# Performance work log

Hardware: AMD Instinct MI355X
Metric: run time of the kernel (lower is better)

## Reference

```python
import jax, jax.numpy as jnp
import numpy as np

N = 4096
IN_F = 256
OUT_F = 64
K = 4
ALPHA = 0.2  # LeakyReLU negative slope
NEG_INF = -9e15


def setup_inputs() -> dict:
    key = jax.random.key(0)
    k_h, k_w, k_a, k_e, k_m = jax.random.split(key, 5)
    h = jax.random.normal(k_h, (N, IN_F), dtype=jnp.float32)
    # xavier_uniform with gain=1.414
    def xavier(k, shape, gain=1.414):
        fan_in, fan_out = shape[0], shape[1]
        limit = gain * np.sqrt(6.0 / (fan_in + fan_out))
        return jax.random.uniform(k, shape, jnp.float32, -limit, limit)
    W = xavier(k_w, (IN_F, OUT_F))
    a = xavier(k_a, (2 * OUT_F, 1))
    vals = jax.random.uniform(k_e, (K, N, N), dtype=jnp.float32)
    mask = jax.random.uniform(k_m, (K, N, N), dtype=jnp.float32) < 0.05
    edge_attr = jnp.where(mask, vals, 0.0)
    return {"h": h, "edge_attr": edge_attr, "W": W, "a": a}


def reference(h, edge_attr, W, a):
    # h: [N, IN_F], edge_attr: [K, N, N], W: [IN_F, OUT_F], a: [2*OUT_F, 1]
    Wh = h @ W                                   # [N, OUT_F]
    Wh1 = Wh @ a[:OUT_F, :]                      # [N, 1]
    Wh2 = Wh @ a[OUT_F:, :]                      # [N, 1]
    e = jax.nn.leaky_relu(Wh1 + Wh2.T, negative_slope=ALPHA)  # [N, N]
    e = e[None, :, :] * edge_attr                # [K, N, N]
    e = jnp.where(edge_attr > 0, e, NEG_INF)
    att = jax.nn.softmax(e, axis=1)              # softmax over dim=1, as in torch
    # dropout is identity in eval mode
    # batched replacement for the per-channel python loop of matmuls
    hp = jnp.einsum('kij,jf->kif', att, Wh)      # [K, N, OUT_F]
    out = jnp.transpose(hp, (1, 0, 2)).reshape(N, K * OUT_F)  # concat dim=1
    return jax.nn.elu(out), att
```

## Files before the change

### kernel.cpp

```cpp
#include <hip/hip_runtime.h>

#define NN 4096
#define IN_F 256
#define OUT_F 64
#define K_CH 4
#define ALPHA 0.2f
#define JP 16
#define JCOLS 256
#define ROWS1 32
#define IC1 128
#define BSTRIDE 264

typedef __bf16 bf16;
typedef __attribute__((ext_vector_type(8))) __bf16 bf16x8;
typedef __attribute__((ext_vector_type(4))) __bf16 bf16x4;
typedef __attribute__((ext_vector_type(4))) float f32x4;

__global__ __launch_bounds__(256) void k0_wh(const float* __restrict__ h,
                                             const float* __restrict__ W,
                                             const float* __restrict__ a,
                                             float* __restrict__ Wh,
                                             float* __restrict__ Wh1,
                                             float* __restrict__ Wh2) {
    int tid = threadIdx.x;
    int wave = tid >> 6, lane = tid & 63;
    int i = blockIdx.x * 4 + wave;
    const float* hrow = h + (size_t)i * IN_F;
    float acc = 0.f;
    #pragma unroll 8
    for (int c = 0; c < IN_F; ++c)
        acc += hrow[c] * W[c * OUT_F + lane];
    Wh[(size_t)i * OUT_F + lane] = acc;
    float v1 = acc * a[lane];
    float v2 = acc * a[OUT_F + lane];
    #pragma unroll
    for (int o = 32; o > 0; o >>= 1) {
        v1 += __shfl_xor(v1, o, 64);
        v2 += __shfl_xor(v2, o, 64);
    }
    if (lane == 0) { Wh1[i] = v1; Wh2[i] = v2; }
}

__global__ __launch_bounds__(256) void k0_transpose(const float* __restrict__ Wh,
                                                    bf16* __restrict__ WhT) {
    __shared__ float lds[OUT_F * 65];
    int tid = threadIdx.x;
    int i0 = blockIdx.x * 64;
    int f = tid & 63;
    int r0 = tid >> 6;
    #pragma unroll
    for (int s = 0; s < 16; ++s) {
        int r = r0 * 16 + s;
        lds[f * 65 + r] = Wh[(size_t)(i0 + r) * OUT_F + f];
    }
    __syncthreads();
    int f2 = tid >> 2;
    int c0 = (tid & 3) * 16;
    #pragma unroll
    for (int s = 0; s < 16; ++s) {
        int c = c0 + s;
        WhT[(size_t)f2 * NN + i0 + c] = (bf16)lds[f2 * 65 + c];
    }
}

__global__ __launch_bounds__(256) void k1_colsum(const float* __restrict__ edge,
                                                 const float* __restrict__ Wh1,
                                                 const float* __restrict__ Wh2,
                                                 bf16* __restrict__ p_buf,
                                                 float* __restrict__ partial) {
    int tid = threadIdx.x;
    int kch = blockIdx.z;
    int j0 = blockIdx.y * 1024 + tid * 4;
    int ic = blockIdx.x;
    int ibase = ic * ROWS1;
    f32x4 w2 = *(const f32x4*)&Wh2[j0];
    f32x4 s = {0.f, 0.f, 0.f, 0.f};
    const float* base = edge + ((size_t)kch * NN + ibase) * NN + j0;
    bf16* pbase = p_buf + ((size_t)kch * NN + ibase) * NN + j0;
    f32x4 r[8];
    #pragma unroll
    for (int t = 0; t < 8; ++t)
        r[t] = *(const f32x4*)(base + (size_t)t * NN);
    #pragma unroll
    for (int ii = 0; ii < ROWS1; ++ii) {
        int cur = ii & 7;
        f32x4 e = r[cur];
        int ip = (ii + 8 < ROWS1) ? ii + 8 : ii;
        r[cur] = *(const f32x4*)(base + (size_t)ip * NN);
        float wh1 = Wh1[ibase + ii];
        bf16x4 pv;
        #pragma unroll
        for (int c = 0; c < 4; ++c) {
            float xv = wh1 + w2[c];
            float lk = xv > 0.f ? xv : ALPHA * xv;
            float val = e[c] > 0.f ? __expf(lk * e[c]) : 0.f;
            bf16 vb = (bf16)val;
            pv[c] = vb;
            s[c] += (float)vb;
        }
        *(bf16x4*)(pbase + (size_t)ii * NN) = pv;
    }
    *(f32x4*)(partial + ((size_t)kch * IC1 + ic) * NN + j0) = s;
}

__global__ __launch_bounds__(256) void k1_reduce(const float* __restrict__ partial,
                                                 float* __restrict__ s_inv) {
    __shared__ float red[256];
    int tid = threadIdx.x;
    int kch = blockIdx.y;
    int jl = tid & 63, g = tid >> 6;
    int j = blockIdx.x * 64 + jl;
    const float* pb = partial + (size_t)kch * IC1 * NN;
    float s = 0.f;
    #pragma unroll 8
    for (int t = 0; t < IC1 / 4; ++t)
        s += pb[(size_t)(g * (IC1 / 4) + t) * NN + j];
    red[tid] = s;
    __syncthreads();
    if (tid < 64) {
        float tot = red[tid] + red[tid + 64] + red[tid + 128] + red[tid + 192];
        s_inv[kch * NN + j] = tot > 0.f ? 1.f / tot : 0.f;
    }
}

__global__ __launch_bounds__(256) void k2_fused(const bf16* __restrict__ p_buf,
                                                const float* __restrict__ s_inv,
                                                const bf16* __restrict__ WhT,
                                                float* __restrict__ att_out,
                                                float* __restrict__ hp) {
    __shared__ bf16 ldsB[OUT_F * BSTRIDE];
    __shared__ float lds_inv[JCOLS];
    int tid = threadIdx.x;
    int itile = blockIdx.x;
    int z = blockIdx.y;
    int kch = z >> 4, jp = z & 15;
    int jbase0 = jp * JCOLS;
    {
        int f = tid >> 2, part = (tid & 3) * 64;
        #pragma unroll
        for (int u = 0; u < 8; ++u) {
            bf16x8 v = *(const bf16x8*)(WhT + (size_t)f * NN + jbase0 + part + u * 8);
            *(bf16x8*)&ldsB[f * BSTRIDE + part + u * 8] = v;
        }
        lds_inv[tid] = s_inv[kch * NN + jbase0 + tid];
    }
    __syncthreads();
    int wave = tid >> 6, lane = tid & 63;
    int n16 = lane & 15, quad = lane >> 4;
    int i_row = itile * 64 + wave * 16 + n16;
    const size_t ebase = ((size_t)kch * NN + i_row) * NN + jbase0 + quad * 8;
    const bf16* pptr = p_buf + ebase;
    float* aptr = att_out + ebase;
    f32x4 acc[4] = {};
    bf16x8 pf[4];
    #pragma unroll
    for (int t = 0; t < 4; ++t)
        pf[t] = *(const bf16x8*)(pptr + t * 32);
    #pragma unroll
    for (int s = 0; s < JCOLS / 32; ++s) {
        int cur = s & 3;
        bf16x8 pv = pf[cur];
        int sp = (s + 4 < JCOLS / 32) ? s + 4 : s;
        pf[cur] = *(const bf16x8*)(pptr + sp * 32);
        int jl = s * 32 + quad * 8;
        f32x4 iv0 = *(const f32x4*)&lds_inv[jl];
        f32x4 iv1 = *(const f32x4*)&lds_inv[jl + 4];
        bf16x8 afrag;
        f32x4 av0, av1;
        #pragma unroll
        for (int c = 0; c < 8; ++c) {
            float isc = c < 4 ? iv0[c] : iv1[c - 4];
            float attv = (float)pv[c] * isc;
            afrag[c] = (bf16)attv;
            if (c < 4) av0[c] = attv; else av1[c - 4] = attv;
        }
        *(f32x4*)(aptr + s * 32) = av0;
        *(f32x4*)(aptr + s * 32 + 4) = av1;
        #pragma unroll
        for (int ft = 0; ft < 4; ++ft) {
            bf16x8 bfrag = *(const bf16x8*)&ldsB[(ft * 16 + n16) * BSTRIDE + jl];
            acc[ft] = __builtin_amdgcn_mfma_f32_16x16x32_bf16(afrag, bfrag, acc[ft], 0, 0, 0);
        }
    }
    #pragma unroll
    for (int ft = 0; ft < 4; ++ft) {
        #pragma unroll
        for (int r = 0; r < 4; ++r) {
            int row_l = quad * 4 + r;
            int i_g = itile * 64 + wave * 16 + row_l;
            size_t idx = ((size_t)z * NN + i_g) * OUT_F + ft * 16 + n16;
            hp[idx] = acc[ft][r];
        }
    }
}

__global__ __launch_bounds__(256) void k3_combine(const float* __restrict__ hp,
                                                  float* __restrict__ out) {
    int g = blockIdx.x * 256 + threadIdx.x;
    int i = g >> 8;
    int rem = g & 255;
    int kch = rem >> 6;
    int f = rem & 63;
    float s = 0.f;
    #pragma unroll
    for (int z = 0; z < JP; ++z)
        s += hp[(((size_t)(kch * JP + z)) * NN + i) * OUT_F + f];
    out[g] = s > 0.f ? s : __expf(s) - 1.f;
}

extern "C" void kernel_launch(void* const* d_in, const int* in_sizes, int n_in,
                              void* d_out, int out_size, void* d_ws, size_t ws_size,
                              hipStream_t stream) {
    (void)out_size; (void)ws_size;
    const float *h = nullptr, *edge = nullptr, *W = nullptr, *a = nullptr;
    for (int i = 0; i < n_in; ++i) {
        int sz = in_sizes[i];
        if (sz == NN * IN_F)               h    = (const float*)d_in[i];
        else if (sz == K_CH * NN * NN)     edge = (const float*)d_in[i];
        else if (sz == IN_F * OUT_F)       W    = (const float*)d_in[i];
        else if (sz == 2 * OUT_F)          a    = (const float*)d_in[i];
    }

    char* ws = (char*)d_ws;
    size_t off = 0;
    float* Wh      = (float*)(ws + off); off += (size_t)NN * OUT_F * 4;
    float* Wh1     = (float*)(ws + off); off += NN * 4;
    float* Wh2     = (float*)(ws + off); off += NN * 4;
    float* s_inv   = (float*)(ws + off); off += (size_t)K_CH * NN * 4;
    bf16*  WhT     = (bf16*) (ws + off); off += (size_t)OUT_F * NN * 2;
    float* partial = (float*)(ws + off); off += (size_t)K_CH * IC1 * NN * 4;
    float* hp      = (float*)(ws + off); off += (size_t)K_CH * JP * NN * OUT_F * 4;
    bf16*  p_buf   = (bf16*) (ws + off); off += (size_t)K_CH * NN * NN * 2;

    float* out_h   = (float*)d_out;
    float* att_out = out_h + (size_t)NN * (K_CH * OUT_F);

    k0_wh<<<dim3(NN / 4), 256, 0, stream>>>(h, W, a, Wh, Wh1, Wh2);
    k0_transpose<<<dim3(NN / 64), 256, 0, stream>>>(Wh, WhT);
    k1_colsum<<<dim3(IC1, 4, K_CH), 256, 0, stream>>>(edge, Wh1, Wh2, p_buf, partial);
    k1_reduce<<<dim3(NN / 64, K_CH), 256, 0, stream>>>(partial, s_inv);
    k2_fused<<<dim3(64, K_CH * JP), 256, 0, stream>>>(p_buf, s_inv, WhT, att_out, hp);
    k3_combine<<<dim3((NN * K_CH * OUT_F) / 256), 256, 0, stream>>>(hp, out_h);
}
```

Before: 593.9 us.

## Fuse split-j partial reduction and ELU into attention-matmul kernel

The attention-times-Wh kernel now loops over the full j range inside each block, staging Wh^T in 256-column LDS slabs, instead of splitting j across 16 blocks. It applies ELU and writes the final output directly. This removes the large partial-sum hp buffer, its write and read-back traffic, and the separate combine launch. In exchange the grid shrinks from 4096 to 256 blocks, roughly one per CU. That low occupancy, plus the per-slab barriers, may leave the memory-bound attention streaming under-saturated.

```diff
diff --git a/kernel.cpp b/kernel.cpp
--- a/kernel.cpp
+++ b/kernel.cpp
@@ -5,8 +5,6 @@
 #define OUT_F 64
 #define K_CH 4
 #define ALPHA 0.2f
-#define JP 16
-#define JCOLS 256
 #define ROWS1 32
 #define IC1 128
 #define BSTRIDE 264
@@ -127,59 +125,63 @@
                                                 const float* __restrict__ s_inv,
                                                 const bf16* __restrict__ WhT,
                                                 float* __restrict__ att_out,
-                                                float* __restrict__ hp) {
+                                                float* __restrict__ out) {
     __shared__ bf16 ldsB[OUT_F * BSTRIDE];
-    __shared__ float lds_inv[JCOLS];
+    __shared__ float lds_inv[NN];
     int tid = threadIdx.x;
     int itile = blockIdx.x;
-    int z = blockIdx.y;
-    int kch = z >> 4, jp = z & 15;
-    int jbase0 = jp * JCOLS;
-    {
-        int f = tid >> 2, part = (tid & 3) * 64;
-        #pragma unroll
-        for (int u = 0; u < 8; ++u) {
-            bf16x8 v = *(const bf16x8*)(WhT + (size_t)f * NN + jbase0 + part + u * 8);
-            *(bf16x8*)&ldsB[f * BSTRIDE + part + u * 8] = v;
-        }
-        lds_inv[tid] = s_inv[kch * NN + jbase0 + tid];
-    }
-    __syncthreads();
+    int kch = blockIdx.y;
+    #pragma unroll
+    for (int t = 0; t < NN / 256; ++t)
+        lds_inv[t * 256 + tid] = s_inv[kch * NN + t * 256 + tid];
     int wave = tid >> 6, lane = tid & 63;
     int n16 = lane & 15, quad = lane >> 4;
     int i_row = itile * 64 + wave * 16 + n16;
-    const size_t ebase = ((size_t)kch * NN + i_row) * NN + jbase0 + quad * 8;
+    const size_t ebase = ((size_t)kch * NN + i_row) * NN + quad * 8;
     const bf16* pptr = p_buf + ebase;
     float* aptr = att_out + ebase;
     f32x4 acc[4] = {};
-    bf16x8 pf[4];
-    #pragma unroll
-    for (int t = 0; t < 4; ++t)
+    bf16x8 pf[8];
+    #pragma unroll
+    for (int t = 0; t < 8; ++t)
         pf[t] = *(const bf16x8*)(pptr + t * 32);
-    #pragma unroll
-    for (int s = 0; s < JCOLS / 32; ++s) {
-        int cur = s & 3;
-        bf16x8 pv = pf[cur];
-        int sp = (s + 4 < JCOLS / 32) ? s + 4 : s;
-        pf[cur] = *(const bf16x8*)(pptr + sp * 32);
-        int jl = s * 32 + quad * 8;
-        f32x4 iv0 = *(const f32x4*)&lds_inv[jl];
-        f32x4 iv1 = *(const f32x4*)&lds_inv[jl + 4];
-        bf16x8 afrag;
-        f32x4 av0, av1;
-        #pragma unroll
-        for (int c = 0; c < 8; ++c) {
-            float isc = c < 4 ? iv0[c] : iv1[c - 4];
-            float attv = (float)pv[c] * isc;
-            afrag[c] = (bf16)attv;
-            if (c < 4) av0[c] = attv; else av1[c - 4] = attv;
-        }
-        *(f32x4*)(aptr + s * 32) = av0;
-        *(f32x4*)(aptr + s * 32 + 4) = av1;
-        #pragma unroll
-        for (int ft = 0; ft < 4; ++ft) {
-            bf16x8 bfrag = *(const bf16x8*)&ldsB[(ft * 16 + n16) * BSTRIDE + jl];
-            acc[ft] = __builtin_amdgcn_mfma_f32_16x16x32_bf16(afrag, bfrag, acc[ft], 0, 0, 0);
+    int f = tid >> 2, part = (tid & 3) * 64;
+    const bf16* wsrc = WhT + (size_t)f * NN + part;
+    for (int slab = 0; slab < 16; ++slab) {
+        __syncthreads();
+        #pragma unroll
+        for (int u = 0; u < 8; ++u) {
+            bf16x8 v = *(const bf16x8*)(wsrc + slab * 256 + u * 8);
+            *(bf16x8*)&ldsB[f * BSTRIDE + part + u * 8] = v;
+        }
+        __syncthreads();
+        #pragma unroll
+        for (int t = 0; t < 8; ++t) {
+            int g = slab * 8 + t;
+            int cur = g & 7;
+            bf16x8 pv = pf[cur];
+            int gp = (g + 8 < 128) ? g + 8 : g;
+            pf[cur] = *(const bf16x8*)(pptr + gp * 32);
+            int jg = g * 32 + quad * 8;
+            int jl = t * 32 + quad * 8;
+            f32x4 iv0 = *(const f32x4*)&lds_inv[jg];
+            f32x4 iv1 = *(const f32x4*)&lds_inv[jg + 4];
+            bf16x8 afrag;
+            f32x4 av0, av1;
+            #pragma unroll
+            for (int c = 0; c < 8; ++c) {
+                float isc = c < 4 ? iv0[c] : iv1[c - 4];
+                float attv = (float)pv[c] * isc;
+                afrag[c] = (bf16)attv;
+                if (c < 4) av0[c] = attv; else av1[c - 4] = attv;
+            }
+            *(f32x4*)(aptr + g * 32) = av0;
+            *(f32x4*)(aptr + g * 32 + 4) = av1;
+            #pragma unroll
+            for (int ft = 0; ft < 4; ++ft) {
+                bf16x8 bfrag = *(const bf16x8*)&ldsB[(ft * 16 + n16) * BSTRIDE + jl];
+                acc[ft] = __builtin_amdgcn_mfma_f32_16x16x32_bf16(afrag, bfrag, acc[ft], 0, 0, 0);
+            }
         }
     }
     #pragma unroll
@@ -188,24 +190,11 @@
         for (int r = 0; r < 4; ++r) {
             int row_l = quad * 4 + r;
             int i_g = itile * 64 + wave * 16 + row_l;
-            size_t idx = ((size_t)z * NN + i_g) * OUT_F + ft * 16 + n16;
-            hp[idx] = acc[ft][r];
-        }
-    }
-}
-
-__global__ __launch_bounds__(256) void k3_combine(const float* __restrict__ hp,
-                                                  float* __restrict__ out) {
-    int g = blockIdx.x * 256 + threadIdx.x;
-    int i = g >> 8;
-    int rem = g & 255;
-    int kch = rem >> 6;
-    int f = rem & 63;
-    float s = 0.f;
-    #pragma unroll
-    for (int z = 0; z < JP; ++z)
-        s += hp[(((size_t)(kch * JP + z)) * NN + i) * OUT_F + f];
-    out[g] = s > 0.f ? s : __expf(s) - 1.f;
+            float v = acc[ft][r];
+            out[(size_t)i_g * (K_CH * OUT_F) + kch * OUT_F + ft * 16 + n16] =
+                v > 0.f ? v : __expf(v) - 1.f;
+        }
+    }
 }
 
 extern "C" void kernel_launch(void* const* d_in, const int* in_sizes, int n_in,
@@ -229,7 +218,6 @@
     float* s_inv   = (float*)(ws + off); off += (size_t)K_CH * NN * 4;
     bf16*  WhT     = (bf16*) (ws + off); off += (size_t)OUT_F * NN * 2;
     float* partial = (float*)(ws + off); off += (size_t)K_CH * IC1 * NN * 4;
-    float* hp      = (float*)(ws + off); off += (size_t)K_CH * JP * NN * OUT_F * 4;
     bf16*  p_buf   = (bf16*) (ws + off); off += (size_t)K_CH * NN * NN * 2;
 
     float* out_h   = (float*)d_out;
@@ -239,6 +227,5 @@
     k0_transpose<<<dim3(NN / 64), 256, 0, stream>>>(Wh, WhT);
     k1_colsum<<<dim3(IC1, 4, K_CH), 256, 0, stream>>>(edge, Wh1, Wh2, p_buf, partial);
     k1_reduce<<<dim3(NN / 64, K_CH), 256, 0, stream>>>(partial, s_inv);
-    k2_fused<<<dim3(64, K_CH * JP), 256, 0, stream>>>(p_buf, s_inv, WhT, att_out, hp);
-    k3_combine<<<dim3((NN * K_CH * OUT_F) / 256), 256, 0, stream>>>(hp, out_h);
-}
+    k2_fused<<<dim3(64, K_CH), 256, 0, stream>>>(p_buf, s_inv, WhT, att_out, out_h);
+}
```

Measured after the change: 591.3 us. Within noise of the previous version (-0.4%).
